# Kernel optimization log

Measured on AMD Instinct MI355X. Metric: run time of the kernel, lower is better.

Reference implementation:

```python
import jax, jax.numpy as jnp
import numpy as np

N, E, F_IN, H, OUT, G = 40000, 640000, 128, 128, 10, 256


def setup_inputs() -> dict:
    key = jax.random.key(0)
    ks = jax.random.split(key, 8)
    x = jax.random.normal(ks[0], (N, F_IN), dtype=jnp.float32)
    edge_index = jax.random.randint(ks[1], (2, E), 0, N, dtype=jnp.int32)
    batch = jnp.sort(jax.random.randint(ks[2], (N,), 0, G, dtype=jnp.int32))
    W1 = jax.random.normal(ks[3], (F_IN, H), dtype=jnp.float32) / np.sqrt(F_IN)
    b1 = jnp.zeros((H,), dtype=jnp.float32)
    W2 = jax.random.normal(ks[4], (H, H), dtype=jnp.float32) / np.sqrt(H)
    b2 = jnp.zeros((H,), dtype=jnp.float32)
    Wfc = jax.random.normal(ks[5], (H, OUT), dtype=jnp.float32) / np.sqrt(H)
    bfc = jnp.zeros((OUT,), dtype=jnp.float32)
    return {"x": x, "edge_index": edge_index, "batch": batch,
            "W1": W1, "b1": b1, "W2": W2, "b2": b2, "Wfc": Wfc, "bfc": bfc}


def _gcn_conv(x, W, b, row, col, num_nodes):
    # x' = D^{-1/2} (A+I) D^{-1/2} (x W) + b   (self-loops already in row/col)
    xw = x @ W                                            # [N, H]
    ones = jnp.ones(row.shape[0], dtype=x.dtype)
    deg = jax.ops.segment_sum(ones, col, num_segments=num_nodes)
    dinv = jnp.where(deg > 0, jax.lax.rsqrt(jnp.maximum(deg, 1.0)), 0.0)
    norm = dinv[row] * dinv[col]                          # [E+N]
    msg = xw[row] * norm[:, None]                         # gather + scale
    return jax.ops.segment_sum(msg, col, num_segments=num_nodes) + b


def reference(x, edge_index, batch, W1, b1, W2, b2, Wfc, bfc):
    num_nodes = x.shape[0]
    loop = jnp.arange(num_nodes, dtype=edge_index.dtype)
    row = jnp.concatenate([edge_index[0], loop])
    col = jnp.concatenate([edge_index[1], loop])

    h = jax.nn.relu(_gcn_conv(x, W1, b1, row, col, num_nodes))
    h = jax.nn.relu(_gcn_conv(h, W2, b2, row, col, num_nodes))

    # global_mean_pool over graph ids
    sums = jax.ops.segment_sum(h, batch, num_segments=G)  # [G, H]
    cnt = jax.ops.segment_sum(jnp.ones(num_nodes, h.dtype), batch, num_segments=G)
    pooled = sums / jnp.maximum(cnt, 1.0)[:, None]

    logits = pooled @ Wfc + bfc                           # [G, OUT]
    return jax.nn.log_softmax(logits, axis=-1)
```

## Files before the change

### kernel.cpp

```cpp
#include <hip/hip_runtime.h>
#include <hip/hip_fp16.h>
#include <math.h>

#define H_DIM 128
#define OUT_DIM 10

typedef __attribute__((ext_vector_type(8))) __bf16 bf16x8;
typedef __attribute__((ext_vector_type(8))) unsigned short ushort8;
typedef __attribute__((ext_vector_type(4))) float f32x4;

__device__ inline unsigned short f2bf_rne(float f) {
    unsigned int u = __float_as_uint(f);
    unsigned int r = u + 0x7FFFu + ((u >> 16) & 1u);
    return (unsigned short)(r >> 16);
}
__device__ inline float bf_lo(unsigned int u) { return __uint_as_float(u << 16); }
__device__ inline float bf_hi(unsigned int u) { return __uint_as_float(u & 0xFFFF0000u); }
__device__ inline float h2f(unsigned int e) {
    return __half2float(__ushort_as_half((unsigned short)(e & 0xFFFFu)));
}

#define ACC4(gv, nv) do { \
    const unsigned int* _u = (const unsigned int*)&(gv); \
    ax[0] += bf_lo(_u[0]) * (nv); ay[0] += bf_hi(_u[0]) * (nv); \
    ax[1] += bf_lo(_u[1]) * (nv); ay[1] += bf_hi(_u[1]) * (nv); \
    ax[2] += bf_lo(_u[2]) * (nv); ay[2] += bf_hi(_u[2]) * (nv); \
    ax[3] += bf_lo(_u[3]) * (nv); ay[3] += bf_hi(_u[3]) * (nv); \
} while (0)

__device__ inline void gather_node(const int4* __restrict__ XW16,
                                   const unsigned int* __restrict__ csr,
                                   int start, int end, int c, float dc2,
                                   int sub, int fl, int lane,
                                   float ax[4], float ay[4]) {
    {
        float s = (sub == 0) ? dc2 : 0.0f;
        int4 gs = XW16[(size_t)c * 16 + fl];
        const unsigned int* u = (const unsigned int*)&gs;
        ax[0] = bf_lo(u[0]) * s; ay[0] = bf_hi(u[0]) * s;
        ax[1] = bf_lo(u[1]) * s; ay[1] = bf_hi(u[1]) * s;
        ax[2] = bf_lo(u[2]) * s; ay[2] = bf_hi(u[2]) * s;
        ax[3] = bf_lo(u[3]) * s; ay[3] = bf_hi(u[3]) * s;
    }
    for (int base = start; base < end; base += 64) {
        int m = end - base; if (m > 64) m = 64;
        unsigned int ce = ((unsigned int)c) << 16;
        if (lane < m) ce = csr[base + lane];
        int groups = (m + 3) >> 2;
        int g = 0;
        for (; g + 3 < groups; g += 4) {
            int j = g * 4 + sub;
            unsigned int e0 = __shfl((int)ce, j);
            unsigned int e1 = __shfl((int)ce, j + 4);
            unsigned int e2 = __shfl((int)ce, j + 8);
            unsigned int e3 = __shfl((int)ce, j + 12);
            int4 g0 = XW16[(size_t)(e0 >> 16) * 16 + fl];
            int4 g1 = XW16[(size_t)(e1 >> 16) * 16 + fl];
            int4 g2 = XW16[(size_t)(e2 >> 16) * 16 + fl];
            int4 g3 = XW16[(size_t)(e3 >> 16) * 16 + fl];
            float n0 = h2f(e0), n1 = h2f(e1), n2 = h2f(e2), n3 = h2f(e3);
            ACC4(g0, n0); ACC4(g1, n1); ACC4(g2, n2); ACC4(g3, n3);
        }
        for (; g < groups; ++g) {
            int j = g * 4 + sub;
            unsigned int e = __shfl((int)ce, j);
            int4 gg = XW16[(size_t)(e >> 16) * 16 + fl];
            float n = h2f(e);
            ACC4(gg, n);
        }
    }
    #pragma unroll
    for (int q = 0; q < 4; ++q) {
        ax[q] += __shfl_xor(ax[q], 16); ax[q] += __shfl_xor(ax[q], 32);
        ay[q] += __shfl_xor(ay[q], 16); ay[q] += __shfl_xor(ay[q], 32);
    }
}

__global__ __launch_bounds__(256) void prep_kernel(const float* __restrict__ W1,
                                                   const float* __restrict__ W2,
                                                   unsigned short* __restrict__ Wt1Hi,
                                                   unsigned short* __restrict__ Wt1Lo,
                                                   unsigned short* __restrict__ Wt2Hi,
                                                   unsigned short* __restrict__ Wt2Lo,
                                                   int hb,
                                                   const int* __restrict__ col,
                                                   int* __restrict__ cnt,
                                                   int* __restrict__ rank, int E) {
    if (blockIdx.x < (unsigned)hb) {
        int e = blockIdx.x * 256 + threadIdx.x;
        if (e < E) rank[e] = atomicAdd(&cnt[col[e]], 1);
    } else {
        int i = (blockIdx.x - hb) * 256 + threadIdx.x;
        const float* src   = (i < 16384) ? W1    : W2;
        unsigned short* dh = (i < 16384) ? Wt1Hi : Wt2Hi;
        unsigned short* dl = (i < 16384) ? Wt1Lo : Wt2Lo;
        int idx = i & 16383;
        int k = idx >> 7, n = idx & 127;
        float v = src[idx];
        unsigned short hbv = f2bf_rne(v);
        float hf = __uint_as_float((unsigned int)hbv << 16);
        unsigned short lb = f2bf_rne(v - hf);
        dh[n * H_DIM + k] = hbv;
        dl[n * H_DIM + k] = lb;
    }
}

__global__ __launch_bounds__(256) void scan_phase1(const int* __restrict__ cnt,
                                                   int* __restrict__ blockSums,
                                                   float* __restrict__ dinv, int N) {
    __shared__ int red[256];
    int base = blockIdx.x * 1024;
    int t = threadIdx.x;
    int s = 0;
    for (int i = 0; i < 4; ++i) {
        int idx = base + t * 4 + i;
        if (idx < N) {
            int cv = cnt[idx];
            s += cv;
            dinv[idx] = rsqrtf((float)cv + 1.0f);
        }
    }
    red[t] = s;
    __syncthreads();
    for (int d = 128; d > 0; d >>= 1) {
        if (t < d) red[t] += red[t + d];
        __syncthreads();
    }
    if (t == 0) blockSums[blockIdx.x] = red[0];
}

__global__ __launch_bounds__(256) void scan_phase23(const int* __restrict__ cnt,
                                                    const int* __restrict__ blockSums,
                                                    int* __restrict__ offs, int N, int B) {
    __shared__ int red[256];
    __shared__ int bsum[256];
    int base = blockIdx.x * 1024;
    int t = threadIdx.x;

    bsum[t] = (t < B && t < (int)blockIdx.x) ? blockSums[t] : 0;

    int v[4];
    int s = 0;
    for (int i = 0; i < 4; ++i) {
        int idx = base + t * 4 + i;
        v[i] = (idx < N) ? cnt[idx] : 0;
        s += v[i];
    }
    red[t] = s;
    __syncthreads();
    for (int d = 128; d > 0; d >>= 1) {
        if (t < d) bsum[t] += bsum[t + d];
        __syncthreads();
    }
    for (int d = 1; d < 256; d <<= 1) {
        int x = (t >= d) ? red[t - d] : 0;
        __syncthreads();
        red[t] += x;
        __syncthreads();
    }
    int run = bsum[0] + ((t == 0) ? 0 : red[t - 1]);
    for (int i = 0; i < 4; ++i) {
        int idx = base + t * 4 + i;
        if (idx < N) { offs[idx] = run; run += v[i]; }
    }
    if ((int)blockIdx.x == B - 1 && t == 255) offs[N] = run;
}

__global__ __launch_bounds__(256) void scatter_gemm1(
        const int* __restrict__ row, const int* __restrict__ col,
        const int* __restrict__ rank, const float* __restrict__ dinv,
        const int* __restrict__ offs, unsigned int* __restrict__ csr, int E, int sb,
        const float* __restrict__ Xf,
        const unsigned short* __restrict__ WtHi, const unsigned short* __restrict__ WtLo,
        unsigned short* __restrict__ Yb, int N) {
    if (blockIdx.x < (unsigned)sb) {
        int e = blockIdx.x * 256 + threadIdx.x;
        if (e >= E) return;
        int r = row[e], c = col[e], rk = rank[e];
        int pos = offs[c] + rk;
        float norm = dinv[r] * dinv[c];
        unsigned short nb = __half_as_ushort(__float2half(norm));
        csr[pos] = (((unsigned int)r) << 16) | nb;
        return;
    }
    int blk  = blockIdx.x - sb;
    int lane = threadIdx.x & 63;
    int wv   = threadIdx.x >> 6;
    int m16  = lane & 15;
    int quad = lane >> 4;
    int nodeBase = blk * 32;

    f32x4 acc[2][2] = {};

    #pragma unroll
    for (int kt = 0; kt < 4; ++kt) {
        int k0 = kt * 32 + quad * 8;

        ushort8 aHi[2], aLo[2];
        #pragma unroll
        for (int mi = 0; mi < 2; ++mi) {
            int node = nodeBase + mi * 16 + m16;
            if (node >= N) node = N - 1;
            const float* p = Xf + (size_t)node * H_DIM + k0;
            f32x4 u = *(const f32x4*)p;
            f32x4 w = *(const f32x4*)(p + 4);
            float vv[8] = {u.x, u.y, u.z, u.w, w.x, w.y, w.z, w.w};
            #pragma unroll
            for (int j = 0; j < 8; ++j) {
                unsigned short hbv = f2bf_rne(vv[j]);
                aHi[mi][j] = hbv;
                aLo[mi][j] = f2bf_rne(vv[j] - __uint_as_float((unsigned int)hbv << 16));
            }
        }

        ushort8 bHi[2], bLo[2];
        #pragma unroll
        for (int ni = 0; ni < 2; ++ni) {
            int n = (wv * 2 + ni) * 16 + m16;
            size_t off = (size_t)n * H_DIM + k0;
            bHi[ni] = *(const ushort8*)(WtHi + off);
            bLo[ni] = *(const ushort8*)(WtLo + off);
        }

        #pragma unroll
        for (int mi = 0; mi < 2; ++mi)
            #pragma unroll
            for (int ni = 0; ni < 2; ++ni) {
                acc[mi][ni] = __builtin_amdgcn_mfma_f32_16x16x32_bf16(
                    __builtin_bit_cast(bf16x8, aHi[mi]),
                    __builtin_bit_cast(bf16x8, bHi[ni]), acc[mi][ni], 0, 0, 0);
                acc[mi][ni] = __builtin_amdgcn_mfma_f32_16x16x32_bf16(
                    __builtin_bit_cast(bf16x8, aLo[mi]),
                    __builtin_bit_cast(bf16x8, bHi[ni]), acc[mi][ni], 0, 0, 0);
                acc[mi][ni] = __builtin_amdgcn_mfma_f32_16x16x32_bf16(
                    __builtin_bit_cast(bf16x8, aHi[mi]),
                    __builtin_bit_cast(bf16x8, bLo[ni]), acc[mi][ni], 0, 0, 0);
            }
    }

    #pragma unroll
    for (int mi = 0; mi < 2; ++mi)
        #pragma unroll
        for (int r = 0; r < 4; ++r) {
            int node = nodeBase + mi * 16 + quad * 4 + r;
            if (node < N) {
                #pragma unroll
                for (int ni = 0; ni < 2; ++ni) {
                    int c = (wv * 2 + ni) * 16 + m16;
                    Yb[(size_t)node * H_DIM + c] = f2bf_rne(acc[mi][ni][r]);
                }
            }
        }
}

__global__ __launch_bounds__(512, 8) void agg1_gemm2(
        const unsigned short* __restrict__ XWb,
        const float* __restrict__ dinv,
        const unsigned int* __restrict__ csr,
        const int* __restrict__ offs,
        const float* __restrict__ bias,
        const unsigned short* __restrict__ WtHi,
        const unsigned short* __restrict__ WtLo,
        unsigned short* __restrict__ Yb,
        int N) {
    __shared__ __align__(16) unsigned short hrow[16][136];
    int lane = threadIdx.x & 63;
    int wv   = threadIdx.x >> 6;
    int sub  = lane >> 4;
    int fl   = lane & 15;
    int nodeBase = blockIdx.x * 8;
    int c = nodeBase + wv;
    const int4* XW16 = (const int4*)XWb;

    float ax[4] = {}, ay[4] = {};
    if (c < N) {
        int start = offs[c], end = offs[c + 1];
        float dc = dinv[c];
        gather_node(XW16, csr, start, end, c, dc * dc, sub, fl, lane, ax, ay);
        float4 b0 = ((const float4*)bias)[fl * 2];
        float4 b1 = ((const float4*)bias)[fl * 2 + 1];
        ax[0] = fmaxf(ax[0] + b0.x, 0.f); ay[0] = fmaxf(ay[0] + b0.y, 0.f);
        ax[1] = fmaxf(ax[1] + b0.z, 0.f); ay[1] = fmaxf(ay[1] + b0.w, 0.f);
        ax[2] = fmaxf(ax[2] + b1.x, 0.f); ay[2] = fmaxf(ay[2] + b1.y, 0.f);
        ax[3] = fmaxf(ax[3] + b1.z, 0.f); ay[3] = fmaxf(ay[3] + b1.w, 0.f);
    }
    if (sub == 0) {
        unsigned int o[4];
        #pragma unroll
        for (int q = 0; q < 4; ++q)
            o[q] = (unsigned int)f2bf_rne(ax[q]) | ((unsigned int)f2bf_rne(ay[q]) << 16);
        *(int4*)&hrow[wv][fl * 8] = *(const int4*)o;
        int4 z; z.x = 0; z.y = 0; z.z = 0; z.w = 0;
        *(int4*)&hrow[wv + 8][fl * 8] = z;
    }
    __syncthreads();

    int m16  = lane & 15;
    int quad = lane >> 4;
    f32x4 acc = {};
    #pragma unroll
    for (int kt = 0; kt < 4; ++kt) {
        int k0 = kt * 32 + quad * 8;
        ushort8 a = *(const ushort8*)&hrow[m16][k0];
        int n = wv * 16 + m16;
        size_t off = (size_t)n * H_DIM + k0;
        ushort8 bHi = *(const ushort8*)(WtHi + off);
        ushort8 bLo = *(const ushort8*)(WtLo + off);
        acc = __builtin_amdgcn_mfma_f32_16x16x32_bf16(
            __builtin_bit_cast(bf16x8, a), __builtin_bit_cast(bf16x8, bHi), acc, 0, 0, 0);
        acc = __builtin_amdgcn_mfma_f32_16x16x32_bf16(
            __builtin_bit_cast(bf16x8, a), __builtin_bit_cast(bf16x8, bLo), acc, 0, 0, 0);
    }
    #pragma unroll
    for (int r = 0; r < 4; ++r) {
        int rw = quad * 4 + r;
        if (rw < 8) {
            int node = nodeBase + rw;
            if (node < N)
                Yb[(size_t)node * H_DIM + wv * 16 + m16] = f2bf_rne(acc[r]);
        }
    }
}

__global__ __launch_bounds__(256) void agg_pool(const unsigned short* __restrict__ XWb,
                                                const float* __restrict__ dinv,
                                                const unsigned int* __restrict__ csr,
                                                const int* __restrict__ offs,
                                                const float* __restrict__ bias,
                                                const int* __restrict__ batch,
                                                float* __restrict__ pooledSum, int N) {
    int wave = (blockIdx.x * 256 + threadIdx.x) >> 6;
    int lane = threadIdx.x & 63;
    int wv   = threadIdx.x >> 6;
    int sub  = lane >> 4;
    int fl   = lane & 15;
    bool active = wave < N;

    float ax[4] = {}, ay[4] = {};
    int c = wave;
    if (active) {
        int start = offs[c], end = offs[c + 1];
        float dc = dinv[c];
        gather_node((const int4*)XWb, csr, start, end, c, dc * dc, sub, fl, lane, ax, ay);
        float4 b0 = ((const float4*)bias)[fl * 2];
        float4 b1 = ((const float4*)bias)[fl * 2 + 1];
        ax[0] = fmaxf(ax[0] + b0.x, 0.f); ay[0] = fmaxf(ay[0] + b0.y, 0.f);
        ax[1] = fmaxf(ax[1] + b0.z, 0.f); ay[1] = fmaxf(ay[1] + b0.w, 0.f);
        ax[2] = fmaxf(ax[2] + b1.x, 0.f); ay[2] = fmaxf(ay[2] + b1.y, 0.f);
        ax[3] = fmaxf(ax[3] + b1.z, 0.f); ay[3] = fmaxf(ay[3] + b1.w, 0.f);
    }

    __shared__ float lacc[4][H_DIM];
    __shared__ int lg[4];
    if (lane == 0) lg[wv] = active ? batch[c] : -1;
    if (sub == 0) {
        float4 f0; f0.x = ax[0]; f0.y = ay[0]; f0.z = ax[1]; f0.w = ay[1];
        float4 f1; f1.x = ax[2]; f1.y = ay[2]; f1.z = ax[3]; f1.w = ay[3];
        ((float4*)&lacc[wv][fl * 8])[0] = f0;
        ((float4*)&lacc[wv][fl * 8])[1] = f1;
    }
    __syncthreads();
    int t = threadIdx.x;
    if (t < H_DIM) {
        float s = 0.f; int cur = -1;
        #pragma unroll
        for (int w = 0; w < 4; ++w) {
            int g = lg[w];
            if (g < 0) continue;
            if (g != cur) {
                if (cur >= 0) atomicAdd(&pooledSum[cur * H_DIM + t], s);
                s = 0.f; cur = g;
            }
            s += lacc[w][t];
        }
        if (cur >= 0) atomicAdd(&pooledSum[cur * H_DIM + t], s);
    }
}

__global__ __launch_bounds__(64) void head_kernel(const float* __restrict__ pooledSum,
                                                  const int* __restrict__ batch,
                                                  const float* __restrict__ Wfc,
                                                  const float* __restrict__ bfc,
                                                  float* __restrict__ out, int N) {
    __shared__ float sl[OUT_DIM + 2];
    __shared__ int bounds[2];
    int g = blockIdx.x;
    int j = threadIdx.x;
    if (j < 2) {
        int v = g + j;
        int lo = 0, hi = N;
        while (lo < hi) {
            int mid = (lo + hi) >> 1;
            if (batch[mid] < v) lo = mid + 1; else hi = mid;
        }
        bounds[j] = lo;
    }
    __syncthreads();
    int cnt = bounds[1] - bounds[0];
    float inv = 1.0f / (float)(cnt > 0 ? cnt : 1);
    if (j < OUT_DIM) {
        float acc = 0.f;
        const float* p = pooledSum + g * H_DIM;
        for (int k = 0; k < H_DIM; ++k) acc += p[k] * Wfc[k * OUT_DIM + j];
        sl[j] = acc * inv + bfc[j];
    }
    __syncthreads();
    if (j == 0) {
        float m = sl[0];
        for (int i = 1; i < OUT_DIM; ++i) m = fmaxf(m, sl[i]);
        float s = 0.f;
        for (int i = 0; i < OUT_DIM; ++i) s += expf(sl[i] - m);
        sl[OUT_DIM] = m + logf(s);
    }
    __syncthreads();
    if (j < OUT_DIM) out[g * OUT_DIM + j] = sl[j] - sl[OUT_DIM];
}

extern "C" void kernel_launch(void* const* d_in, const int* in_sizes, int n_in,
                              void* d_out, int out_size, void* d_ws, size_t ws_size,
                              hipStream_t stream) {
    const float* x     = (const float*)d_in[0];
    const int*   ei    = (const int*)  d_in[1];
    const int*   batch = (const int*)  d_in[2];
    const float* W1    = (const float*)d_in[3];
    const float* b1    = (const float*)d_in[4];
    const float* W2    = (const float*)d_in[5];
    const float* b2    = (const float*)d_in[6];
    const float* Wfc   = (const float*)d_in[7];
    const float* bfc   = (const float*)d_in[8];
    float* out = (float*)d_out;

    int N = in_sizes[2];
    int E = in_sizes[1] / 2;
    int G = out_size / OUT_DIM;
    const int* row = ei;
    const int* col = ei + E;

    char* wsb = (char*)d_ws;
    size_t nAlign = (size_t)((N + 256) / 256) * 256;
    size_t eAlign = (size_t)((E + 255) / 256) * 256;
    int*   cnt       = (int*)wsb;
    float* pooledSum = (float*)(cnt + nAlign);
    int*   offs      = (int*)(pooledSum + (size_t)G * H_DIM);
    int*   rank      = offs + nAlign;
    float* dinv      = (float*)(rank + eAlign);
    unsigned int* csr = (unsigned int*)(dinv + nAlign);
    unsigned short* Xb = (unsigned short*)(csr + eAlign);
    unsigned short* Hb = Xb + (size_t)N * H_DIM;
    int* blockSums = (int*)(Hb + (size_t)N * H_DIM);
    unsigned short* Wt1Hi = (unsigned short*)(blockSums + 256);
    unsigned short* Wt1Lo = Wt1Hi + H_DIM * H_DIM;
    unsigned short* Wt2Hi = Wt1Lo + H_DIM * H_DIM;
    unsigned short* Wt2Lo = Wt2Hi + H_DIM * H_DIM;

    int scanBlocks = (N + 1023) / 1024;
    int histBlocks = (E + 255) / 256;
    int gemmBlocks = (N + 31) / 32;

    hipMemsetAsync(cnt, 0, (nAlign + (size_t)G * H_DIM) * sizeof(int), stream);

    prep_kernel<<<histBlocks + 128, 256, 0, stream>>>(
        W1, W2, Wt1Hi, Wt1Lo, Wt2Hi, Wt2Lo, histBlocks, col, cnt, rank, E);

    scan_phase1<<<scanBlocks, 256, 0, stream>>>(cnt, blockSums, dinv, N);
    scan_phase23<<<scanBlocks, 256, 0, stream>>>(cnt, blockSums, offs, N, scanBlocks);

    scatter_gemm1<<<histBlocks + gemmBlocks, 256, 0, stream>>>(
        row, col, rank, dinv, offs, csr, E, histBlocks,
        x, Wt1Hi, Wt1Lo, Xb, N);

    int ag1Blocks = (N + 7) / 8;
    agg1_gemm2<<<ag1Blocks, 512, 0, stream>>>(Xb, dinv, csr, offs, b1,
                                              Wt2Hi, Wt2Lo, Hb, N);

    int aggBlocks = (N + 3) / 4;
    agg_pool<<<aggBlocks, 256, 0, stream>>>(Hb, dinv, csr, offs, b2,
                                            batch, pooledSum, N);

    head_kernel<<<G, 64, 0, stream>>>(pooledSum, batch, Wfc, bfc, out, N);
}
```

Before: 241.2 us.

## Use edge-parallel LDS-atomic aggregation for layer-2 pooling and retile agg1_gemm2

Replaces the node-per-wave layer-2 aggregation with an edge-parallel kernel. Each 256-thread block covers 32 nodes, walks their CSR edges in flat chunks, binary-searches each edge's destination node and accumulates into shared memory with LDS atomics. The self-loop term, bias, ReLU and graph pooling are applied in an epilogue. agg1_gemm2 now uses 256-thread blocks where each wave gathers 4 nodes, so all 16 MFMA rows are real nodes instead of 8 zero-padded ones, and each wave computes two N-tiles. This aims to balance load across uneven degrees and cut wasted MFMA work, at the cost of LDS atomic contention and less latency hiding per wave.

```diff
diff --git a/kernel.cpp b/kernel.cpp
--- a/kernel.cpp
+++ b/kernel.cpp
@@ -4,6 +4,7 @@
 
 #define H_DIM 128
 #define OUT_DIM 10
+#define NBLK 32
 
 typedef __attribute__((ext_vector_type(8))) __bf16 bf16x8;
 typedef __attribute__((ext_vector_type(8))) unsigned short ushort8;
@@ -253,7 +254,7 @@
         }
 }
 
-__global__ __launch_bounds__(512, 8) void agg1_gemm2(
+__global__ __launch_bounds__(256) void agg1_gemm2(
         const unsigned short* __restrict__ XWb,
         const float* __restrict__ dinv,
         const unsigned int* __restrict__ csr,
@@ -268,113 +269,193 @@
     int wv   = threadIdx.x >> 6;
     int sub  = lane >> 4;
     int fl   = lane & 15;
-    int nodeBase = blockIdx.x * 8;
-    int c = nodeBase + wv;
+    int nodeBase = blockIdx.x * 16;
     const int4* XW16 = (const int4*)XWb;
-
-    float ax[4] = {}, ay[4] = {};
-    if (c < N) {
-        int start = offs[c], end = offs[c + 1];
-        float dc = dinv[c];
-        gather_node(XW16, csr, start, end, c, dc * dc, sub, fl, lane, ax, ay);
-        float4 b0 = ((const float4*)bias)[fl * 2];
-        float4 b1 = ((const float4*)bias)[fl * 2 + 1];
-        ax[0] = fmaxf(ax[0] + b0.x, 0.f); ay[0] = fmaxf(ay[0] + b0.y, 0.f);
-        ax[1] = fmaxf(ax[1] + b0.z, 0.f); ay[1] = fmaxf(ay[1] + b0.w, 0.f);
-        ax[2] = fmaxf(ax[2] + b1.x, 0.f); ay[2] = fmaxf(ay[2] + b1.y, 0.f);
-        ax[3] = fmaxf(ax[3] + b1.z, 0.f); ay[3] = fmaxf(ay[3] + b1.w, 0.f);
-    }
-    if (sub == 0) {
-        unsigned int o[4];
-        #pragma unroll
-        for (int q = 0; q < 4; ++q)
-            o[q] = (unsigned int)f2bf_rne(ax[q]) | ((unsigned int)f2bf_rne(ay[q]) << 16);
-        *(int4*)&hrow[wv][fl * 8] = *(const int4*)o;
-        int4 z; z.x = 0; z.y = 0; z.z = 0; z.w = 0;
-        *(int4*)&hrow[wv + 8][fl * 8] = z;
+    float4 b0 = ((const float4*)bias)[fl * 2];
+    float4 b1 = ((const float4*)bias)[fl * 2 + 1];
+
+    for (int i = 0; i < 4; ++i) {
+        int c = nodeBase + wv * 4 + i;
+        float ax[4] = {}, ay[4] = {};
+        if (c < N) {
+            int start = offs[c], end = offs[c + 1];
+            float dc = dinv[c];
+            gather_node(XW16, csr, start, end, c, dc * dc, sub, fl, lane, ax, ay);
+            ax[0] = fmaxf(ax[0] + b0.x, 0.f); ay[0] = fmaxf(ay[0] + b0.y, 0.f);
+            ax[1] = fmaxf(ax[1] + b0.z, 0.f); ay[1] = fmaxf(ay[1] + b0.w, 0.f);
+            ax[2] = fmaxf(ax[2] + b1.x, 0.f); ay[2] = fmaxf(ay[2] + b1.y, 0.f);
+            ax[3] = fmaxf(ax[3] + b1.z, 0.f); ay[3] = fmaxf(ay[3] + b1.w, 0.f);
+        }
+        if (sub == 0) {
+            unsigned int o[4];
+            #pragma unroll
+            for (int q = 0; q < 4; ++q)
+                o[q] = (unsigned int)f2bf_rne(ax[q]) | ((unsigned int)f2bf_rne(ay[q]) << 16);
+            *(int4*)&hrow[wv * 4 + i][fl * 8] = *(const int4*)o;
+        }
     }
     __syncthreads();
 
     int m16  = lane & 15;
     int quad = lane >> 4;
-    f32x4 acc = {};
+    f32x4 acc[2] = {};
     #pragma unroll
     for (int kt = 0; kt < 4; ++kt) {
         int k0 = kt * 32 + quad * 8;
         ushort8 a = *(const ushort8*)&hrow[m16][k0];
-        int n = wv * 16 + m16;
-        size_t off = (size_t)n * H_DIM + k0;
-        ushort8 bHi = *(const ushort8*)(WtHi + off);
-        ushort8 bLo = *(const ushort8*)(WtLo + off);
-        acc = __builtin_amdgcn_mfma_f32_16x16x32_bf16(
-            __builtin_bit_cast(bf16x8, a), __builtin_bit_cast(bf16x8, bHi), acc, 0, 0, 0);
-        acc = __builtin_amdgcn_mfma_f32_16x16x32_bf16(
-            __builtin_bit_cast(bf16x8, a), __builtin_bit_cast(bf16x8, bLo), acc, 0, 0, 0);
+        #pragma unroll
+        for (int ni = 0; ni < 2; ++ni) {
+            int n = (wv * 2 + ni) * 16 + m16;
+            size_t off = (size_t)n * H_DIM + k0;
+            ushort8 bHi = *(const ushort8*)(WtHi + off);
+            ushort8 bLo = *(const ushort8*)(WtLo + off);
+            acc[ni] = __builtin_amdgcn_mfma_f32_16x16x32_bf16(
+                __builtin_bit_cast(bf16x8, a),
+                __builtin_bit_cast(bf16x8, bHi), acc[ni], 0, 0, 0);
+            acc[ni] = __builtin_amdgcn_mfma_f32_16x16x32_bf16(
+                __builtin_bit_cast(bf16x8, a),
+                __builtin_bit_cast(bf16x8, bLo), acc[ni], 0, 0, 0);
+        }
     }
     #pragma unroll
     for (int r = 0; r < 4; ++r) {
-        int rw = quad * 4 + r;
-        if (rw < 8) {
-            int node = nodeBase + rw;
-            if (node < N)
-                Yb[(size_t)node * H_DIM + wv * 16 + m16] = f2bf_rne(acc[r]);
-        }
-    }
-}
-
-__global__ __launch_bounds__(256) void agg_pool(const unsigned short* __restrict__ XWb,
-                                                const float* __restrict__ dinv,
-                                                const unsigned int* __restrict__ csr,
-                                                const int* __restrict__ offs,
-                                                const float* __restrict__ bias,
-                                                const int* __restrict__ batch,
-                                                float* __restrict__ pooledSum, int N) {
-    int wave = (blockIdx.x * 256 + threadIdx.x) >> 6;
-    int lane = threadIdx.x & 63;
-    int wv   = threadIdx.x >> 6;
-    int sub  = lane >> 4;
-    int fl   = lane & 15;
-    bool active = wave < N;
-
-    float ax[4] = {}, ay[4] = {};
-    int c = wave;
-    if (active) {
-        int start = offs[c], end = offs[c + 1];
-        float dc = dinv[c];
-        gather_node((const int4*)XWb, csr, start, end, c, dc * dc, sub, fl, lane, ax, ay);
-        float4 b0 = ((const float4*)bias)[fl * 2];
-        float4 b1 = ((const float4*)bias)[fl * 2 + 1];
-        ax[0] = fmaxf(ax[0] + b0.x, 0.f); ay[0] = fmaxf(ay[0] + b0.y, 0.f);
-        ax[1] = fmaxf(ax[1] + b0.z, 0.f); ay[1] = fmaxf(ay[1] + b0.w, 0.f);
-        ax[2] = fmaxf(ax[2] + b1.x, 0.f); ay[2] = fmaxf(ay[2] + b1.y, 0.f);
-        ax[3] = fmaxf(ax[3] + b1.z, 0.f); ay[3] = fmaxf(ay[3] + b1.w, 0.f);
-    }
-
-    __shared__ float lacc[4][H_DIM];
-    __shared__ int lg[4];
-    if (lane == 0) lg[wv] = active ? batch[c] : -1;
-    if (sub == 0) {
-        float4 f0; f0.x = ax[0]; f0.y = ay[0]; f0.z = ax[1]; f0.w = ay[1];
-        float4 f1; f1.x = ax[2]; f1.y = ay[2]; f1.z = ax[3]; f1.w = ay[3];
-        ((float4*)&lacc[wv][fl * 8])[0] = f0;
-        ((float4*)&lacc[wv][fl * 8])[1] = f1;
-    }
-    __syncthreads();
+        int node = nodeBase + quad * 4 + r;
+        if (node < N) {
+            #pragma unroll
+            for (int ni = 0; ni < 2; ++ni) {
+                int cc = (wv * 2 + ni) * 16 + m16;
+                Yb[(size_t)node * H_DIM + cc] = f2bf_rne(acc[ni][r]);
+            }
+        }
+    }
+}
+
+__global__ __launch_bounds__(256) void agg_pool_ep(const unsigned short* __restrict__ XWb,
+                                                   const float* __restrict__ dinv,
+                                                   const unsigned int* __restrict__ csr,
+                                                   const int* __restrict__ offs,
+                                                   const float* __restrict__ bias,
+                                                   const int* __restrict__ batch,
+                                                   float* __restrict__ pooledSum, int N) {
+    __shared__ float lacc[NBLK][132];
+    __shared__ int   loffs[NBLK + 1];
+    __shared__ int   lbatch[NBLK];
+    __shared__ float ldinv[NBLK];
     int t = threadIdx.x;
-    if (t < H_DIM) {
-        float s = 0.f; int cur = -1;
-        #pragma unroll
-        for (int w = 0; w < 4; ++w) {
-            int g = lg[w];
-            if (g < 0) continue;
-            if (g != cur) {
-                if (cur >= 0) atomicAdd(&pooledSum[cur * H_DIM + t], s);
-                s = 0.f; cur = g;
+    int c0 = blockIdx.x * NBLK;
+
+    for (int i = t; i < NBLK * 132; i += 256) ((float*)lacc)[i] = 0.f;
+    if (t <= NBLK) {
+        int idx = c0 + t; if (idx > N) idx = N;
+        loffs[t] = offs[idx];
+    }
+    if (t < NBLK) {
+        int c = c0 + t;
+        lbatch[t] = (c < N) ? batch[c] : -1;
+        ldinv[t]  = (c < N) ? dinv[c] : 0.f;
+    }
+    __syncthreads();
+
+    int s0 = loffs[0], s1 = loffs[NBLK];
+    int lane = t & 63, wv = t >> 6, sub = lane >> 4, fl = lane & 15;
+    const int4* XW16 = (const int4*)XWb;
+
+    for (int base = s0 + wv * 64; base < s1; base += 256) {
+        int m = s1 - base; if (m > 64) m = 64;
+        unsigned int ce = 0;
+        int cL = 0;
+        if (lane < m) {
+            ce = csr[base + lane];
+            int e = base + lane;
+            int lo = 0, hi = NBLK - 1;
+            #pragma unroll
+            for (int it = 0; it < 5; ++it) {
+                int mid = (lo + hi + 1) >> 1;
+                if (loffs[mid] <= e) lo = mid; else hi = mid - 1;
             }
-            s += lacc[w][t];
-        }
-        if (cur >= 0) atomicAdd(&pooledSum[cur * H_DIM + t], s);
-    }
+            cL = lo;
+        }
+        int groups = (m + 3) >> 2;
+        int g = 0;
+        #define EP_EDGE(ev, cv) do { \
+            int4 gv = XW16[(size_t)((ev) >> 16) * 16 + fl]; \
+            float nn = h2f(ev); \
+            float* L = &lacc[cv][0]; \
+            const unsigned int* u = (const unsigned int*)&gv; \
+            atomicAdd(L + 0 * 16 + fl, bf_lo(u[0]) * nn); \
+            atomicAdd(L + 1 * 16 + fl, bf_hi(u[0]) * nn); \
+            atomicAdd(L + 2 * 16 + fl, bf_lo(u[1]) * nn); \
+            atomicAdd(L + 3 * 16 + fl, bf_hi(u[1]) * nn); \
+            atomicAdd(L + 4 * 16 + fl, bf_lo(u[2]) * nn); \
+            atomicAdd(L + 5 * 16 + fl, bf_hi(u[2]) * nn); \
+            atomicAdd(L + 6 * 16 + fl, bf_lo(u[3]) * nn); \
+            atomicAdd(L + 7 * 16 + fl, bf_hi(u[3]) * nn); \
+        } while (0)
+        for (; g + 3 < groups; g += 4) {
+            int j = g * 4 + sub;
+            unsigned int e0 = __shfl((int)ce, j);      int cj0 = __shfl(cL, j);
+            unsigned int e1 = __shfl((int)ce, j + 4);  int cj1 = __shfl(cL, j + 4);
+            unsigned int e2 = __shfl((int)ce, j + 8);  int cj2 = __shfl(cL, j + 8);
+            unsigned int e3 = __shfl((int)ce, j + 12); int cj3 = __shfl(cL, j + 12);
+            int4 v0 = XW16[(size_t)(e0 >> 16) * 16 + fl];
+            int4 v1 = XW16[(size_t)(e1 >> 16) * 16 + fl];
+            int4 v2 = XW16[(size_t)(e2 >> 16) * 16 + fl];
+            int4 v3 = XW16[(size_t)(e3 >> 16) * 16 + fl];
+            float n0 = h2f(e0), n1 = h2f(e1), n2 = h2f(e2), n3 = h2f(e3);
+            {
+                const unsigned int* u; float* L;
+                u = (const unsigned int*)&v0; L = &lacc[cj0][0];
+                atomicAdd(L + 0*16 + fl, bf_lo(u[0])*n0); atomicAdd(L + 1*16 + fl, bf_hi(u[0])*n0);
+                atomicAdd(L + 2*16 + fl, bf_lo(u[1])*n0); atomicAdd(L + 3*16 + fl, bf_hi(u[1])*n0);
+                atomicAdd(L + 4*16 + fl, bf_lo(u[2])*n0); atomicAdd(L + 5*16 + fl, bf_hi(u[2])*n0);
+                atomicAdd(L + 6*16 + fl, bf_lo(u[3])*n0); atomicAdd(L + 7*16 + fl, bf_hi(u[3])*n0);
+                u = (const unsigned int*)&v1; L = &lacc[cj1][0];
+                atomicAdd(L + 0*16 + fl, bf_lo(u[0])*n1); atomicAdd(L + 1*16 + fl, bf_hi(u[0])*n1);
+                atomicAdd(L + 2*16 + fl, bf_lo(u[1])*n1); atomicAdd(L + 3*16 + fl, bf_hi(u[1])*n1);
+                atomicAdd(L + 4*16 + fl, bf_lo(u[2])*n1); atomicAdd(L + 5*16 + fl, bf_hi(u[2])*n1);
+                atomicAdd(L + 6*16 + fl, bf_lo(u[3])*n1); atomicAdd(L + 7*16 + fl, bf_hi(u[3])*n1);
+                u = (const unsigned int*)&v2; L = &lacc[cj2][0];
+                atomicAdd(L + 0*16 + fl, bf_lo(u[0])*n2); atomicAdd(L + 1*16 + fl, bf_hi(u[0])*n2);
+                atomicAdd(L + 2*16 + fl, bf_lo(u[1])*n2); atomicAdd(L + 3*16 + fl, bf_hi(u[1])*n2);
+                atomicAdd(L + 4*16 + fl, bf_lo(u[2])*n2); atomicAdd(L + 5*16 + fl, bf_hi(u[2])*n2);
+                atomicAdd(L + 6*16 + fl, bf_lo(u[3])*n2); atomicAdd(L + 7*16 + fl, bf_hi(u[3])*n2);
+                u = (const unsigned int*)&v3; L = &lacc[cj3][0];
+                atomicAdd(L + 0*16 + fl, bf_lo(u[0])*n3); atomicAdd(L + 1*16 + fl, bf_hi(u[0])*n3);
+                atomicAdd(L + 2*16 + fl, bf_lo(u[1])*n3); atomicAdd(L + 3*16 + fl, bf_hi(u[1])*n3);
+                atomicAdd(L + 4*16 + fl, bf_lo(u[2])*n3); atomicAdd(L + 5*16 + fl, bf_hi(u[2])*n3);
+                atomicAdd(L + 6*16 + fl, bf_lo(u[3])*n3); atomicAdd(L + 7*16 + fl, bf_hi(u[3])*n3);
+            }
+        }
+        for (; g < groups; ++g) {
+            int j = g * 4 + sub;
+            unsigned int e = __shfl((int)ce, j);
+            int cj = __shfl(cL, j);
+            EP_EDGE(e, cj);
+        }
+        #undef EP_EDGE
+    }
+    __syncthreads();
+
+    int f = t & 127, half = t >> 7;
+    float bsv = bias[f];
+    int pidx = (f & 7) * 16 + (f >> 3);
+    float s = 0.f; int cur = -1;
+    for (int i = 0; i < NBLK / 2; ++i) {
+        int n = half * (NBLK / 2) + i;
+        int c = c0 + n;
+        if (c >= N) break;
+        float dc = ldinv[n];
+        float selfv = __uint_as_float(((unsigned int)XWb[(size_t)c * H_DIM + f]) << 16)
+                      * (dc * dc);
+        float val = fmaxf(lacc[n][pidx] + selfv + bsv, 0.f);
+        int g = lbatch[n];
+        if (g != cur) {
+            if (cur >= 0) atomicAdd(&pooledSum[cur * H_DIM + f], s);
+            s = 0.f; cur = g;
+        }
+        s += val;
+    }
+    if (cur >= 0) atomicAdd(&pooledSum[cur * H_DIM + f], s);
 }
 
 __global__ __launch_bounds__(64) void head_kernel(const float* __restrict__ pooledSum,
@@ -469,13 +550,13 @@
         row, col, rank, dinv, offs, csr, E, histBlocks,
         x, Wt1Hi, Wt1Lo, Xb, N);
 
-    int ag1Blocks = (N + 7) / 8;
-    agg1_gemm2<<<ag1Blocks, 512, 0, stream>>>(Xb, dinv, csr, offs, b1,
+    int ag1Blocks = (N + 15) / 16;
+    agg1_gemm2<<<ag1Blocks, 256, 0, stream>>>(Xb, dinv, csr, offs, b1,
                                               Wt2Hi, Wt2Lo, Hb, N);
 
-    int aggBlocks = (N + 3) / 4;
-    agg_pool<<<aggBlocks, 256, 0, stream>>>(Hb, dinv, csr, offs, b2,
-                                            batch, pooledSum, N);
+    int aggBlocks = (N + NBLK - 1) / NBLK;
+    agg_pool_ep<<<aggBlocks, 256, 0, stream>>>(Hb, dinv, csr, offs, b2,
+                                               batch, pooledSum, N);
 
     head_kernel<<<G, 64, 0, stream>>>(pooledSum, batch, Wfc, bfc, out, N);
 }
```

New measurement: 644.9 us. 167% more time.
